# Optimization experiments

Measured on AMD Instinct MI355X. Metric: run time of the kernel, lower is better.

Reference implementation:

```python
import jax, jax.numpy as jnp
import numpy as np

FS = 512.0
N_PHA = 10
N_AMP = 10
FIR_LEN = 513  # odd, ~1 s at fs=512 -> resolves 2 Hz band edges
N_BINS = 18    # hard-coded in PAC.__init__
TEMP = 0.01    # ModulationIndex temperature (near-hard soft binning)
EPS = 1e-8


def _design_filters():
    # Windowed-sinc FIR bandpass, one kernel per band: h = lp(hi) - lp(lo), Hamming window.
    t = np.arange(FIR_LEN) - (FIR_LEN - 1) / 2.0
    win = np.hamming(FIR_LEN)
    def bp(lo, hi):
        lp = lambda fc: 2.0 * fc / FS * np.sinc(2.0 * fc / FS * t)
        return (lp(hi) - lp(lo)) * win
    pha_c = np.linspace(2.0, 20.0, N_PHA)
    amp_c = np.linspace(60.0, 160.0, N_AMP)
    bands = [(0.75 * c, 1.25 * c) for c in pha_c] + [(0.75 * c, 1.25 * c) for c in amp_c]
    return np.stack([bp(lo, hi) for lo, hi in bands]).astype(np.float32)  # (20, L)


def setup_inputs() -> dict:
    key = jax.random.key(0)
    x = jax.random.normal(key, (4, 16, 4096), dtype=jnp.float32)  # (B, C, T)
    filters = jnp.asarray(_design_filters())                      # (n_pha+n_amp, L)
    return {"x": x, "filters": filters}


def _analytic(sig):
    # FFT-based Hilbert analytic signal along last axis.
    T = sig.shape[-1]
    h = np.zeros(T, np.float32)
    h[0] = 1.0
    if T % 2 == 0:
        h[T // 2] = 1.0
        h[1:T // 2] = 2.0
    else:
        h[1:(T + 1) // 2] = 2.0
    return jnp.fft.ifft(jnp.fft.fft(sig, axis=-1) * jnp.asarray(h), axis=-1)


def reference(x, filters):
    B, C, T = x.shape
    L = filters.shape[-1]
    # Bandpass: (B*C, 1, T) x (n_bands, 1, L) -> (B*C, n_bands, T); symmetric kernels so corr == conv.
    xf = jax.lax.conv_general_dilated(
        x.reshape(-1, 1, T), filters[:, None, :],
        window_strides=(1,), padding=[(L // 2, L // 2)])
    xf = xf.reshape(B, C, -1, T)
    phase = jnp.angle(_analytic(xf[:, :, :N_PHA]))        # (B, C, P, T)
    amplitude = jnp.abs(_analytic(xf[:, :, N_PHA:]))      # (B, C, A, T)
    # Soft circular phase binning (temperature -> near one-hot).
    centers = jnp.asarray((-np.pi + 2.0 * np.pi * (np.arange(N_BINS) + 0.5) / N_BINS).astype(np.float32))
    d = jnp.mod(phase[..., None] - centers + np.pi, 2.0 * np.pi) - np.pi  # (B,C,P,T,K)
    w = jax.nn.softmax(-(d * d) / TEMP, axis=-1)
    # Mean amplitude per phase bin, per (pha, amp) band pair.
    amp_sum = jnp.einsum('bcptk,bcat->bcpak', w, amplitude)  # (B,C,P,A,K)
    cnt = w.sum(axis=-2)                                      # (B,C,P,K)
    mean_amp = amp_sum / (cnt[:, :, :, None, :] + EPS)
    p = mean_amp / (mean_amp.sum(-1, keepdims=True) + EPS)
    log_k = jnp.log(jnp.float32(N_BINS))
    mi = (log_k + (p * jnp.log(p + EPS)).sum(-1)) / log_k    # Tort MI, (B,C,P,A)
    return mi
```

## Files before the change

kernel.cpp:

```cpp
#include <hip/hip_runtime.h>
#include <math.h>

#define T_LEN 4096
#define FIR_L 513
#define N_PHA 10
#define N_AMP 10
#define N_BANDS 20
#define N_BINS 18
#define BC 64

typedef __attribute__((ext_vector_type(8))) short short8;
typedef __attribute__((ext_vector_type(4))) float f32x4;

#define ZA(i) (((i) << 1) + ((((i) >> 4)) << 1))

__device__ float2 twg_dev[1024];

static __device__ __forceinline__ unsigned short f2bf(float x) {
    unsigned u = __float_as_uint(x);
    unsigned r = u + 0x7FFFu + ((u >> 16) & 1u);
    return (unsigned short)(r >> 16);
}

static __device__ __forceinline__ int digitrev12(int p) {
    unsigned rr = __brev((unsigned)p) >> 20;
    rr = ((rr & 0x555u) << 1) | ((rr & 0xAAAu) >> 1);
    return (int)rr;
}

static __device__ __forceinline__ void tw_derive(const float2* tw, int m1,
        float& c1, float& s1, float& c2, float& s2, float& c3, float& s3) {
    const float2 w1 = tw[m1];
    c1 = w1.x; s1 = w1.y;
    s2 = 2.0f * s1 * c1;
    c2 = fmaf(-2.0f * s1, s1, 1.0f);
    c3 = c1 * c2 - s1 * s2;
    s3 = s1 * c2 + c1 * s2;
}

static __device__ __forceinline__ float2 cmul_em(float2 u, float c, float s) {
    return make_float2(u.x * c + u.y * s, u.y * c - u.x * s);
}

static __device__ __forceinline__ void bf_fwd(float2& A, float2& B, float2& C, float2& D,
        float c1, float s1, float c2, float s2, float c3, float s3) {
    const float t0r = A.x + C.x, t0i = A.y + C.y;
    const float t1r = A.x - C.x, t1i = A.y - C.y;
    const float t2r = B.x + D.x, t2i = B.y + D.y;
    const float t3r = B.x - D.x, t3i = B.y - D.y;
    const float y0r = t0r + t2r,  y0i = t0i + t2i;
    const float u1r = t1r + t3i, u1i = t1i - t3r;
    const float u2r = t0r - t2r, u2i = t0i - t2i;
    const float u3r = t1r - t3i, u3i = t1i + t3r;
    A = make_float2(y0r, y0i);
    B = make_float2(u1r * c1 + u1i * s1, u1i * c1 - u1r * s1);
    C = make_float2(u2r * c2 + u2i * s2, u2i * c2 - u2r * s2);
    D = make_float2(u3r * c3 + u3i * s3, u3i * c3 - u3r * s3);
}

static __device__ __forceinline__ void bf_inv(float2& A, float2& B, float2& C, float2& D,
        float c1, float s1, float c2, float s2, float c3, float s3) {
    const float tbr = B.x * c1 - B.y * s1, tbi = B.y * c1 + B.x * s1;
    const float tcr = C.x * c2 - C.y * s2, tci = C.y * c2 + C.x * s2;
    const float tdr = D.x * c3 - D.y * s3, tdi = D.y * c3 + D.x * s3;
    const float ar = A.x, ai = A.y;
    A = make_float2(ar + tbr + tcr + tdr, ai + tbi + tci + tdi);
    B = make_float2(ar - tbi - tcr + tdi, ai + tbr - tci - tdr);
    C = make_float2(ar - tbr + tcr - tdr, ai - tbi + tci - tdi);
    D = make_float2(ar + tbi - tcr - tdi, ai - tbr - tci + tdr);
}

static __device__ __forceinline__ void fft_fwd_passes(float* z, const float2* tw,
                                                      int tid, int s0) {
    for (int s = s0; s < 6; s += 2) {
        const int hl = 10 - 2 * s;
        const int h  = 1 << hl;
        const int h4 = h >> 2;
        const int kk = tid & (h4 - 1);
        const int g  = tid >> (hl - 2);
        const int i0 = (g << (hl + 2)) + kk;
        float2 e[4][4];
#pragma unroll
        for (int j = 0; j < 4; ++j)
#pragma unroll
            for (int r = 0; r < 4; ++r)
                e[j][r] = *(const float2*)&z[ZA(i0 + j * h4 + r * h)];
#pragma unroll
        for (int j = 0; j < 4; ++j) {
            float c1, s1, c2, s2, c3, s3;
            tw_derive(tw, (kk + j * h4) << (2 * s), c1, s1, c2, s2, c3, s3);
            bf_fwd(e[j][0], e[j][1], e[j][2], e[j][3], c1, s1, c2, s2, c3, s3);
        }
        {
            float c1, s1, c2, s2, c3, s3;
            tw_derive(tw, kk << (2 * s + 2), c1, s1, c2, s2, c3, s3);
#pragma unroll
            for (int r = 0; r < 4; ++r)
                bf_fwd(e[0][r], e[1][r], e[2][r], e[3][r], c1, s1, c2, s2, c3, s3);
        }
#pragma unroll
        for (int j = 0; j < 4; ++j)
#pragma unroll
            for (int r = 0; r < 4; ++r)
                *(float2*)&z[ZA(i0 + j * h4 + r * h)] = e[j][r];
        __syncthreads();
    }
}

static __device__ __forceinline__ void fft_fwd_pass1_sparse(
        float* z, const float2* tw, int tid, float2 F, float2 Tl) {
    float c1, s1, c2, s2, c3, s3;
    tw_derive(tw, tid, c1, s1, c2, s2, c3, s3);
    float2 P[4];
    P[0] = F;
    P[1] = cmul_em(F, c1, s1);
    P[2] = cmul_em(F, c2, s2);
    P[3] = cmul_em(F, c3, s3);
    tw_derive(tw, tid + 768, c1, s1, c2, s2, c3, s3);
    const float2 iT  = make_float2(-Tl.y,  Tl.x);
    const float2 nT  = make_float2(-Tl.x, -Tl.y);
    const float2 niT = make_float2( Tl.y, -Tl.x);
    float2 Q[4];
    Q[0] = Tl;
    Q[1] = cmul_em(iT,  c1, s1);
    Q[2] = cmul_em(nT,  c2, s2);
    Q[3] = cmul_em(niT, c3, s3);
    tw_derive(tw, tid << 2, c1, s1, c2, s2, c3, s3);
#pragma unroll
    for (int r = 0; r < 4; ++r) {
        const int ib = tid + (r << 10);
        const float2 A = make_float2(P[r].x + Q[r].x, P[r].y + Q[r].y);
        const float2 B = cmul_em(make_float2(P[r].x - Q[r].y, P[r].y + Q[r].x), c1, s1);
        const float2 C = cmul_em(make_float2(P[r].x - Q[r].x, P[r].y - Q[r].y), c2, s2);
        const float2 D = cmul_em(make_float2(P[r].x + Q[r].y, P[r].y - Q[r].x), c3, s3);
        *(float2*)&z[ZA(ib)]        = A;
        *(float2*)&z[ZA(ib + 256)]  = B;
        *(float2*)&z[ZA(ib + 512)]  = C;
        *(float2*)&z[ZA(ib + 768)]  = D;
    }
}

static __device__ __forceinline__ void fft_inv6(float* z, const float2* tw, int tid) {
#pragma unroll
    for (int s = 0; s < 6; s += 2) {
        const int L  = 1 << (2 * s);
        const int k  = tid & (L - 1);
        const int g  = tid >> (2 * s);
        const int i0 = (g << (2 * s + 4)) + k;
        float2 e[4][4];
#pragma unroll
        for (int j = 0; j < 4; ++j)
#pragma unroll
            for (int r = 0; r < 4; ++r)
                e[j][r] = *(const float2*)&z[ZA(i0 + j * L + (r << (2 * s + 2)))];
        {
            float c1, s1, c2, s2, c3, s3;
            tw_derive(tw, k << (10 - 2 * s), c1, s1, c2, s2, c3, s3);
#pragma unroll
            for (int r = 0; r < 4; ++r)
                bf_inv(e[0][r], e[1][r], e[2][r], e[3][r], c1, s1, c2, s2, c3, s3);
        }
#pragma unroll
        for (int j = 0; j < 4; ++j) {
            float c1, s1, c2, s2, c3, s3;
            tw_derive(tw, (k + j * L) << (8 - 2 * s), c1, s1, c2, s2, c3, s3);
            bf_inv(e[j][0], e[j][1], e[j][2], e[j][3], c1, s1, c2, s2, c3, s3);
        }
#pragma unroll
        for (int j = 0; j < 4; ++j)
#pragma unroll
            for (int r = 0; r < 4; ++r)
                *(float2*)&z[ZA(i0 + j * L + (r << (2 * s + 2)))] = e[j][r];
        __syncthreads();
    }
}

__global__ __launch_bounds__(256) void spectral_pre(
    const float* __restrict__ x,
    const float* __restrict__ filt,
    float2* __restrict__ Xs,
    float2* __restrict__ Hs,
    float* __restrict__ corr)
{
    __shared__ __align__(16) float sm[11265];

    const int tid = threadIdx.x;
    const int b   = blockIdx.x;

    if (b == BC + N_BANDS) {
        for (int m = tid; m < 1024; m += 256) {
            float ang = (float)m * (6.283185307179586f / 4096.0f);
            float s, c;
            sincosf(ang, &s, &c);
            twg_dev[m] = make_float2(c, s);
        }
        return;
    }

    if (b > BC + N_BANDS) {
        const int cidx = b - (BC + N_BANDS + 1);
        const int bc   = cidx >> 3;
        const int oct  = cidx & 7;
        float* xe  = sm;
        float* fbs = sm + 512;

        const float* xrow = x + bc * T_LEN;
        for (int i = tid; i < 512; i += 256)
            xe[i] = (i < 256) ? xrow[i] : xrow[3584 + i];
        for (int i = tid; i < N_BANDS * FIR_L; i += 256)
            fbs[i] = filt[i];
        __syncthreads();

        const int tl = tid & 31;
        const int bg = (tid >> 5) & 3;
        const int t  = oct * 32 + tl;
        if (tid < 128) {
#pragma unroll 1
            for (int b5 = 0; b5 < 5; ++b5) {
                const int band = bg * 5 + b5;
                const float* fbp = fbs + band * FIR_L;
                float cf = 0.0f;
                for (int l = 0; l <= 255 - t; ++l)
                    cf = fmaf(fbp[l], xe[256 + t + l], cf);
                corr[((bc * N_BANDS + band) * 2 + 0) * 256 + t] = cf;
            }
        } else {
#pragma unroll 1
            for (int b5 = 0; b5 < 5; ++b5) {
                const int band = bg * 5 + b5;
                const float* fbp = fbs + band * FIR_L;
                float ct = 0.0f;
                for (int j = 0; j <= t; ++j)
                    ct = fmaf(fbp[512 - t + j], xe[j], ct);
                corr[((bc * N_BANDS + band) * 2 + 1) * 256 + t] = ct;
            }
        }
        return;
    }

    float*  z   = sm;
    float2* twl = (float2*)(sm + 8704);
    float*  fb  = sm + 8704 + 2048;

    for (int m = tid; m < 1024; m += 256) {
        float ang = (float)m * (6.283185307179586f / 4096.0f);
        float s, c;
        sincosf(ang, &s, &c);
        twl[m] = make_float2(c, s);
    }

    if (b < BC) {
        const float* xrow = x + b * T_LEN;
        for (int i = tid; i < 4096; i += 256)
            *(float2*)&z[ZA(i)] = make_float2(xrow[i], 0.0f);
    } else {
        const int band = b - BC;
        for (int i = tid; i < FIR_L; i += 256) fb[i] = filt[band * FIR_L + i];
        __syncthreads();
        for (int i = tid; i < 4096; i += 256) {
            float hv = 0.0f;
            if (i < 257)        hv = fb[256 - i];
            else if (i >= 3840) hv = fb[4352 - i];
            *(float2*)&z[ZA(i)] = make_float2(hv, 0.0f);
        }
    }
    __syncthreads();

    fft_fwd_passes(z, twl, tid, 0);

    float2* dst = (b < BC) ? (Xs + b * 4096) : (Hs + (b - BC) * 4096);
    for (int i = tid; i < 4096; i += 256)
        dst[i] = *(const float2*)&z[ZA(i)];
}

__global__ __launch_bounds__(256, 4) void spectral_main_pre(
    const float* __restrict__ corr,
    const float2* __restrict__ Xs,
    const float2* __restrict__ Hs,
    float* __restrict__ pha,
    unsigned short* __restrict__ amp_bf)
{
    __shared__ __align__(16) float z[8704];

    const int tid  = threadIdx.x;
    const int bc   = blockIdx.x / N_BANDS;
    const int band = blockIdx.x % N_BANDS;
    const float2* tw = twg_dev;

    const float cf = corr[((bc * N_BANDS + band) * 2 + 0) * 256 + tid];
    const float ct = corr[((bc * N_BANDS + band) * 2 + 1) * 256 + tid];

    fft_fwd_pass1_sparse(z, tw, tid, make_float2(-cf, 0.0f), make_float2(-ct, 0.0f));
    __syncthreads();
    fft_fwd_passes(z, tw, tid, 2);

    const float2* Xrow = Xs + bc * 4096;
    const float2* Hrow = Hs + band * 4096;
    for (int i = tid; i < 4096; i += 256) {
        const float2 X = Xrow[i];
        const float2 H = Hrow[i];
        const float2 C = *(const float2*)&z[ZA(i)];
        float pr = X.x * H.x - X.y * H.y + C.x;
        float pi = X.x * H.y + X.y * H.x + C.y;
        const int f = digitrev12(i);
        const float mf = (f == 0 || f == 2048) ? 1.0f : (f < 2048 ? 2.0f : 0.0f);
        *(float2*)&z[ZA(i)] = make_float2(pr * mf, pi * mf);
    }
    __syncthreads();

    fft_inv6(z, tw, tid);

    const float inv_n = 1.0f / 4096.0f;
    if (band < N_PHA) {
        float* dst = pha + (bc * N_PHA + band) * T_LEN;
        for (int i = tid; i < 4096; i += 256) {
            const float2 zz = *(const float2*)&z[ZA(i)];
            dst[i] = atan2f(zz.y, zz.x);
        }
    } else {
        unsigned short* dst = amp_bf + (bc * N_AMP + (band - N_PHA)) * T_LEN;
        for (int i = tid; i < 4096; i += 256) {
            const float2 zz = *(const float2*)&z[ZA(i)];
            dst[i] = f2bf(sqrtf(zz.x * zz.x + zz.y * zz.y) * inv_n);
        }
    }
}

__global__ __launch_bounds__(256, 4) void spectral_main_inline(
    const float* __restrict__ x,
    const float* __restrict__ filt,
    const float2* __restrict__ Xs,
    const float2* __restrict__ Hs,
    float* __restrict__ pha,
    unsigned short* __restrict__ amp_bf)
{
    __shared__ float z[8704];
    __shared__ float xe[512];
    __shared__ float fb[FIR_L];

    const int tid  = threadIdx.x;
    const int bc   = blockIdx.x / N_BANDS;
    const int band = blockIdx.x % N_BANDS;
    const float2* tw = twg_dev;

    const float* xrow = x + bc * T_LEN;
    for (int i = tid; i < 512; i += 256)
        xe[i] = (i < 256) ? xrow[i] : xrow[3584 + i];
    for (int i = tid; i < FIR_L; i += 256) fb[i] = filt[band * FIR_L + i];
    __syncthreads();

    float cf = 0.0f, ct = 0.0f;
    for (int l = 0; l <= 255 - tid; ++l)
        cf = fmaf(fb[l], xe[256 + tid + l], cf);
    for (int j = 0; j <= tid; ++j)
        ct = fmaf(fb[512 - tid + j], xe[j], ct);

    fft_fwd_pass1_sparse(z, tw, tid, make_float2(-cf, 0.0f), make_float2(-ct, 0.0f));
    __syncthreads();
    fft_fwd_passes(z, tw, tid, 2);

    const float2* Xrow = Xs + bc * 4096;
    const float2* Hrow = Hs + band * 4096;
    for (int i = tid; i < 4096; i += 256) {
        const float2 X = Xrow[i];
        const float2 H = Hrow[i];
        const float2 C = *(const float2*)&z[ZA(i)];
        float pr = X.x * H.x - X.y * H.y + C.x;
        float pi = X.x * H.y + X.y * H.x + C.y;
        const int f = digitrev12(i);
        const float mf = (f == 0 || f == 2048) ? 1.0f : (f < 2048 ? 2.0f : 0.0f);
        *(float2*)&z[ZA(i)] = make_float2(pr * mf, pi * mf);
    }
    __syncthreads();

    fft_inv6(z, tw, tid);

    const float inv_n = 1.0f / 4096.0f;
    if (band < N_PHA) {
        float* dst = pha + (bc * N_PHA + band) * T_LEN;
        for (int i = tid; i < 4096; i += 256) {
            const float2 zz = *(const float2*)&z[ZA(i)];
            dst[i] = atan2f(zz.y, zz.x);
        }
    } else {
        unsigned short* dst = amp_bf + (bc * N_AMP + (band - N_PHA)) * T_LEN;
        for (int i = tid; i < 4096; i += 256) {
            const float2 zz = *(const float2*)&z[ZA(i)];
            dst[i] = f2bf(sqrtf(zz.x * zz.x + zz.y * zz.y) * inv_n);
        }
    }
}

__global__ __launch_bounds__(512) void bin_mi_mfma(
    const float* __restrict__ pha,
    const unsigned short* __restrict__ amp_bf,
    float* __restrict__ out)
{
    const int tid  = threadIdx.x;
    const int lane = tid & 63;
    const int wv   = tid >> 6;
    const int bc   = blockIdx.x / N_PHA;
    const int p    = blockIdx.x % N_PHA;

    __shared__ unsigned int wbufW[8][18 * 68];
    __shared__ float psum[8][11][N_BINS];
    __shared__ float asum[11][N_BINS];

    const float* phrow = pha + (bc * N_PHA + p) * T_LEN;
    const unsigned short* arow = amp_bf + bc * N_AMP * T_LEN;

    const float PI_F  = 3.14159274101257324f;
    const float INVD  = 2.8647889756541160f;
    const float DELTA = 0.34906585039886590f;
    const float C1    = 12.184696791468343f;
    const float C2    = 69.813170079773180f;

    const int m_ = lane & 15;
    const int q_ = lane >> 4;
    const int n_ = lane & 15;

    short8 zero8;
#pragma unroll
    for (int j = 0; j < 8; ++j) zero8[j] = 0;
    short8 ones8;
#pragma unroll
    for (int j = 0; j < 8; ++j) ones8[j] = (short)0x3F80;

    f32x4 acc0 = {0.f, 0.f, 0.f, 0.f};
    f32x4 acc1 = {0.f, 0.f, 0.f, 0.f};

    const int base_t = wv * 512;
    unsigned short* wh = (unsigned short*)&wbufW[wv][0];

    float2 pp[4];
#pragma unroll
    for (int c = 0; c < 4; ++c)
        pp[c] = *(const float2*)&phrow[base_t + c * 128 + lane * 2];

    for (int chunk = 0; chunk < 4; ++chunk) {
        const int cb = base_t + chunk * 128;

        short8 af[4];
#pragma unroll
        for (int s = 0; s < 4; ++s) {
            const int tA = cb + s * 32 + q_ * 8;
            if (m_ < N_AMP)       af[s] = *(const short8*)(arow + m_ * T_LEN + tA);
            else if (m_ == N_AMP) af[s] = ones8;
            else                  af[s] = zero8;
        }

#pragma unroll
        for (int k = 0; k < N_BINS; ++k)
            wbufW[wv][k * 68 + lane] = 0u;

#pragma unroll
        for (int h = 0; h < 2; ++h) {
            const float ph = h ? pp[chunk].y : pp[chunk].x;
            float u  = (ph + PI_F) * INVD;
            float jf = floorf(u);
            float d  = (u - jf - 0.5f) * DELTA;
            int j0 = (int)jf;
            if (j0 >= N_BINS) j0 -= N_BINS;
            const int jm = (j0 == 0) ? N_BINS - 1 : j0 - 1;
            const int jp = (j0 == N_BINS - 1) ? 0 : j0 + 1;
            const float em = expf(-C1 - C2 * d);
            const float ep = expf(-C1 + C2 * d);
            const float inv = 1.0f / (1.0f + em + ep);
            wh[(j0 * 68 + lane) * 2 + h] = f2bf(inv);
            wh[(jm * 68 + lane) * 2 + h] = f2bf(em * inv);
            wh[(jp * 68 + lane) * 2 + h] = f2bf(ep * inv);
        }
        __builtin_amdgcn_wave_barrier();

#pragma unroll
        for (int s = 0; s < 4; ++s) {
            const int woff = s * 16 + q_ * 4;
            short8 bfrag0 = *(const short8*)&wbufW[wv][n_ * 68 + woff];
            short8 bfrag1 = (n_ < 2)
                ? *(const short8*)&wbufW[wv][(16 + n_) * 68 + woff]
                : zero8;
            acc0 = __builtin_amdgcn_mfma_f32_16x16x32_bf16(af[s], bfrag0, acc0, 0, 0, 0);
            acc1 = __builtin_amdgcn_mfma_f32_16x16x32_bf16(af[s], bfrag1, acc1, 0, 0, 0);
        }
        __builtin_amdgcn_wave_barrier();
    }

#pragma unroll
    for (int r = 0; r < 4; ++r) {
        const int m = q_ * 4 + r;
        if (m < 11) {
            psum[wv][m][n_] = acc0[r];
            if (n_ < 2) psum[wv][m][16 + n_] = acc1[r];
        }
    }
    __syncthreads();

    if (tid < 11 * N_BINS) {
        const int m = tid / N_BINS;
        const int k = tid % N_BINS;
        float s = 0.0f;
#pragma unroll
        for (int w = 0; w < 8; ++w) s += psum[w][m][k];
        asum[m][k] = s;
    }
    __syncthreads();

    if (tid < N_AMP) {
        float ma[N_BINS];
        float msum = 0.0f;
#pragma unroll
        for (int k = 0; k < N_BINS; ++k) {
            float m = asum[tid][k] / (asum[10][k] + 1e-8f);
            ma[k] = m;
            msum += m;
        }
        const float inv = 1.0f / (msum + 1e-8f);
        float acc = 0.0f;
#pragma unroll
        for (int k = 0; k < N_BINS; ++k) {
            float pk = ma[k] * inv;
            acc = fmaf(pk, logf(pk + 1e-8f), acc);
        }
        const float logk = 2.89037175789124f;
        out[(bc * N_PHA + p) * N_AMP + tid] = (logk + acc) / logk;
    }
}

extern "C" void kernel_launch(void* const* d_in, const int* in_sizes, int n_in,
                              void* d_out, int out_size, void* d_ws, size_t ws_size,
                              hipStream_t stream) {
    const float* x    = (const float*)d_in[0];
    const float* filt = (const float*)d_in[1];
    float* out = (float*)d_out;

    float* pha = (float*)d_ws;
    unsigned short* amp_bf = (unsigned short*)(pha + BC * N_PHA * T_LEN);
    float2* Xs = (float2*)(amp_bf + BC * N_AMP * T_LEN);
    float2* Hs = Xs + BC * 4096;
    float* corr = (float*)(Hs + N_BANDS * 4096);

    const size_t need = (size_t)BC * N_PHA * T_LEN * 4
                      + (size_t)BC * N_AMP * T_LEN * 2
                      + (size_t)BC * 4096 * 8
                      + (size_t)N_BANDS * 4096 * 8
                      + (size_t)BC * N_BANDS * 2 * 256 * 4;
    const bool fits = (ws_size >= need);

    if (fits) {
        spectral_pre<<<BC + N_BANDS + 1 + 512, 256, 0, stream>>>(x, filt, Xs, Hs, corr);
        spectral_main_pre<<<BC * N_BANDS, 256, 0, stream>>>(corr, Xs, Hs, pha, amp_bf);
    } else {
        spectral_pre<<<BC + N_BANDS + 1, 256, 0, stream>>>(x, filt, Xs, Hs, corr);
        spectral_main_inline<<<BC * N_BANDS, 256, 0, stream>>>(x, filt, Xs, Hs, pha, amp_bf);
    }
    bin_mi_mfma<<<BC * N_PHA, 512, 0, stream>>>(pha, amp_bf, out);
}
```

Baseline: 121.9 us.

## Regrid correction blocks per band, skip zero Hilbert bins, use polynomial atan2

The edge-correction blocks in spectral_pre now run one block per (channel, band) with each thread computing both correction sums, instead of eight blocks per channel that each stage all 20 filters. The spectrum-multiply loop replaces the digit-reverse mask computation with index-pattern logic: it writes zeros directly into the negative-frequency slots without loading X, H or C, so those global loads are skipped. Phase extraction swaps the library atan2f for a minimax-polynomial approximation. The changes aim to cut staging work, global loads and transcendental cost, but the custom atan2 adds small error and the index-pattern logic relies on a particular slot ordering.

```diff
diff --git a/kernel.cpp b/kernel.cpp
--- a/kernel.cpp
+++ b/kernel.cpp
@@ -22,10 +22,23 @@
     return (unsigned short)(r >> 16);
 }
 
-static __device__ __forceinline__ int digitrev12(int p) {
-    unsigned rr = __brev((unsigned)p) >> 20;
-    rr = ((rr & 0x555u) << 1) | ((rr & 0xAAAu) >> 1);
-    return (int)rr;
+static __device__ __forceinline__ float fast_atan2f(float y, float x) {
+    const float ax = fabsf(x), ay = fabsf(y);
+    const float mx = fmaxf(ax, ay), mn = fminf(ax, ay);
+    const bool swap = ay > ax;
+    const bool red  = mn > 0.4142135623730950f * mx;
+    const float num = red ? (mn - mx) : mn;
+    const float den = red ? (mn + mx) : mx;
+    const float u  = num / den;
+    const float z2 = u * u;
+    float p = fmaf(8.05374449538e-2f, z2, -1.38776856032e-1f);
+    p = fmaf(p, z2, 1.99777106478e-1f);
+    p = fmaf(p, z2, -3.33329491539e-1f);
+    float a = fmaf(p * z2, u, u);
+    if (red)  a += 0.7853981633974483f;
+    if (swap) a = 1.5707963267948966f - a;
+    if (x < 0.0f) a = 3.14159265358979323f - a;
+    return (y < 0.0f) ? -a : a;
 }
 
 static __device__ __forceinline__ void tw_derive(const float2* tw, int m1,
@@ -199,42 +212,27 @@
 
     if (b > BC + N_BANDS) {
         const int cidx = b - (BC + N_BANDS + 1);
-        const int bc   = cidx >> 3;
-        const int oct  = cidx & 7;
-        float* xe  = sm;
-        float* fbs = sm + 512;
+        const int bc   = cidx / N_BANDS;
+        const int band = cidx % N_BANDS;
+        float* xe = sm;
+        float* fb = sm + 512;
 
         const float* xrow = x + bc * T_LEN;
         for (int i = tid; i < 512; i += 256)
             xe[i] = (i < 256) ? xrow[i] : xrow[3584 + i];
-        for (int i = tid; i < N_BANDS * FIR_L; i += 256)
-            fbs[i] = filt[i];
+        for (int i = tid; i < FIR_L; i += 256)
+            fb[i] = filt[band * FIR_L + i];
         __syncthreads();
 
-        const int tl = tid & 31;
-        const int bg = (tid >> 5) & 3;
-        const int t  = oct * 32 + tl;
-        if (tid < 128) {
-#pragma unroll 1
-            for (int b5 = 0; b5 < 5; ++b5) {
-                const int band = bg * 5 + b5;
-                const float* fbp = fbs + band * FIR_L;
-                float cf = 0.0f;
-                for (int l = 0; l <= 255 - t; ++l)
-                    cf = fmaf(fbp[l], xe[256 + t + l], cf);
-                corr[((bc * N_BANDS + band) * 2 + 0) * 256 + t] = cf;
-            }
-        } else {
-#pragma unroll 1
-            for (int b5 = 0; b5 < 5; ++b5) {
-                const int band = bg * 5 + b5;
-                const float* fbp = fbs + band * FIR_L;
-                float ct = 0.0f;
-                for (int j = 0; j <= t; ++j)
-                    ct = fmaf(fbp[512 - t + j], xe[j], ct);
-                corr[((bc * N_BANDS + band) * 2 + 1) * 256 + t] = ct;
-            }
-        }
+        const int t = tid;
+        float cf = 0.0f, ct = 0.0f;
+        for (int l = 0; l <= 255 - t; ++l)
+            cf = fmaf(fb[l], xe[256 + t + l], cf);
+        for (int j = 0; j <= t; ++j)
+            ct = fmaf(fb[512 - t + j], xe[j], ct);
+
+        corr[((bc * N_BANDS + band) * 2 + 0) * 256 + t] = cf;
+        corr[((bc * N_BANDS + band) * 2 + 1) * 256 + t] = ct;
         return;
     }
 
@@ -296,15 +294,31 @@
 
     const float2* Xrow = Xs + bc * 4096;
     const float2* Hrow = Hs + band * 4096;
-    for (int i = tid; i < 4096; i += 256) {
+#pragma unroll
+    for (int k = 0; k < 8; ++k) {
+        const int s = tid + (k << 8);
+        const int i = ((s >> 1) << 2) | (s & 1);
         const float2 X = Xrow[i];
         const float2 H = Hrow[i];
         const float2 C = *(const float2*)&z[ZA(i)];
-        float pr = X.x * H.x - X.y * H.y + C.x;
-        float pi = X.x * H.y + X.y * H.x + C.y;
-        const int f = digitrev12(i);
-        const float mf = (f == 0 || f == 2048) ? 1.0f : (f < 2048 ? 2.0f : 0.0f);
+        const float pr = X.x * H.x - X.y * H.y + C.x;
+        const float pi = X.x * H.y + X.y * H.x + C.y;
+        const float mf = (i == 0) ? 1.0f : 2.0f;
         *(float2*)&z[ZA(i)] = make_float2(pr * mf, pi * mf);
+    }
+#pragma unroll
+    for (int k = 0; k < 8; ++k) {
+        const int s = tid + (k << 8);
+        const int i = ((s >> 1) << 2) | 2 | (s & 1);
+        if (i == 2) {
+            const float2 X = Xrow[2];
+            const float2 H = Hrow[2];
+            const float2 C = *(const float2*)&z[ZA(2)];
+            *(float2*)&z[ZA(2)] = make_float2(X.x * H.x - X.y * H.y + C.x,
+                                              X.x * H.y + X.y * H.x + C.y);
+        } else {
+            *(float2*)&z[ZA(i)] = make_float2(0.0f, 0.0f);
+        }
     }
     __syncthreads();
 
@@ -315,7 +329,7 @@
         float* dst = pha + (bc * N_PHA + band) * T_LEN;
         for (int i = tid; i < 4096; i += 256) {
             const float2 zz = *(const float2*)&z[ZA(i)];
-            dst[i] = atan2f(zz.y, zz.x);
+            dst[i] = fast_atan2f(zz.y, zz.x);
         }
     } else {
         unsigned short* dst = amp_bf + (bc * N_AMP + (band - N_PHA)) * T_LEN;
@@ -367,8 +381,8 @@
         const float2 C = *(const float2*)&z[ZA(i)];
         float pr = X.x * H.x - X.y * H.y + C.x;
         float pi = X.x * H.y + X.y * H.x + C.y;
-        const int f = digitrev12(i);
-        const float mf = (f == 0 || f == 2048) ? 1.0f : (f < 2048 ? 2.0f : 0.0f);
+        const int m4 = i & 3;
+        const float mf = (i == 0 || i == 2) ? 1.0f : (m4 < 2 ? 2.0f : 0.0f);
         *(float2*)&z[ZA(i)] = make_float2(pr * mf, pi * mf);
     }
     __syncthreads();
@@ -380,7 +394,7 @@
         float* dst = pha + (bc * N_PHA + band) * T_LEN;
         for (int i = tid; i < 4096; i += 256) {
             const float2 zz = *(const float2*)&z[ZA(i)];
-            dst[i] = atan2f(zz.y, zz.x);
+            dst[i] = fast_atan2f(zz.y, zz.x);
         }
     } else {
         unsigned short* dst = amp_bf + (bc * N_AMP + (band - N_PHA)) * T_LEN;
@@ -547,7 +561,7 @@
     const bool fits = (ws_size >= need);
 
     if (fits) {
-        spectral_pre<<<BC + N_BANDS + 1 + 512, 256, 0, stream>>>(x, filt, Xs, Hs, corr);
+        spectral_pre<<<BC + N_BANDS + 1 + BC * N_BANDS, 256, 0, stream>>>(x, filt, Xs, Hs, corr);
         spectral_main_pre<<<BC * N_BANDS, 256, 0, stream>>>(corr, Xs, Hs, pha, amp_bf);
     } else {
         spectral_pre<<<BC + N_BANDS + 1, 256, 0, stream>>>(x, filt, Xs, Hs, corr);
```

Result: faster. 115.3 us, median of 2 (-5.4%).
